# Kernel tuning notes

Hardware: AMD Instinct MI355X
Metric: run time of the kernel (lower is better)

Reference implementation:

```python
import jax, jax.numpy as jnp
import numpy as np
import math

B, S, D, H = 4, 2048, 1024, 16
HD = D // H
WINDOW = 86400.0 * 7.0  # 7 days, per create_time_mask(window_size=...)


def setup_inputs() -> dict:
    key = jax.random.key(0)
    ks = jax.random.split(key, 12)
    x = jax.random.normal(ks[0], (B, S, D), dtype=jnp.float32)
    # transaction timestamps: uniform over 30 days, sorted per sequence
    timestamps = jnp.sort(jax.random.uniform(ks[1], (B, S), dtype=jnp.float32) * (86400.0 * 30.0), axis=-1)
    init = 0.02
    Wq = jax.random.normal(ks[2], (D, D), dtype=jnp.float32) * init
    bq = jnp.zeros((D,), dtype=jnp.float32)
    Wk = jax.random.normal(ks[3], (D, D), dtype=jnp.float32) * init
    bk = jnp.zeros((D,), dtype=jnp.float32)
    Wv = jax.random.normal(ks[4], (D, D), dtype=jnp.float32) * init
    bv = jnp.zeros((D,), dtype=jnp.float32)
    Wo = jax.random.normal(ks[5], (D, D), dtype=jnp.float32) * init
    bo = jnp.zeros((D,), dtype=jnp.float32)
    Wc = jax.random.normal(ks[6], (1, D), dtype=jnp.float32) * init
    bc = jnp.zeros((1,), dtype=jnp.float32)
    return {"x": x, "timestamps": timestamps, "Wq": Wq, "bq": bq, "Wk": Wk, "bk": bk,
            "Wv": Wv, "bv": bv, "Wo": Wo, "bo": bo, "Wc": Wc, "bc": bc}


def reference(x, timestamps, Wq, bq, Wk, bk, Wv, bv, Wo, bo, Wc, bc):
    b, s, d = x.shape
    scale = 1.0 / math.sqrt(HD)
    # projections (torch Linear: y = x @ W.T + b), split heads -> [b, s, H, HD]
    Q = (x @ Wq.T + bq).reshape(b, s, H, HD)
    K = (x @ Wk.T + bk).reshape(b, s, H, HD)
    V = (x @ Wv.T + bv).reshape(b, s, H, HD)
    # scores [b, H, q, k]
    scores = jnp.einsum('bqhd,bkhd->bhqk', Q, K) * scale
    # time-window mask: attend only within +/- WINDOW seconds
    time_mask = jnp.abs(timestamps[:, :, None] - timestamps[:, None, :]) <= WINDOW  # [b, s, s]
    scores = jnp.where(time_mask[:, None, :, :], scores, -jnp.inf)
    attn = jax.nn.softmax(scores, axis=-1)
    attended = jnp.einsum('bhqk,bkhd->bqhd', attn, V).reshape(b, s, d)
    output = attended @ Wo.T + bo
    change_scores = (output @ Wc.T + bc)[..., 0]  # [b, s]
    return output, change_scores
```

## Files before the change

kernel.cpp:

```cpp
#include <hip/hip_runtime.h>
#include <math.h>

#define BB 4
#define SS 2048
#define DD 1024
#define HH 16
#define HDD 64
#define NN (BB*SS)
#define WINDOWF 604800.0f
#define LOG2E 1.44269504088896340736f
#define SCALE2 (0.125f * LOG2E)
#define MSTATIC 24.0f

typedef __attribute__((ext_vector_type(8))) short bf16x8;
typedef __attribute__((ext_vector_type(4))) short bf16x4;
typedef __attribute__((ext_vector_type(4))) short s16x4;
typedef __attribute__((ext_vector_type(4))) float f32x4;

__device__ __forceinline__ unsigned short f2b(float f) {
    unsigned int x = __float_as_uint(f);
    unsigned int r = x + 0x7FFFu + ((x >> 16) & 1u);
    return (unsigned short)(r >> 16);
}

__device__ __forceinline__ unsigned int cvt_pk_bf16(float lo, float hi) {
    unsigned int r;
    asm("v_cvt_pk_bf16_f32 %0, %1, %2" : "=v"(r) : "v"(lo), "v"(hi));
    return r;
}

__device__ __forceinline__ void gload16(const unsigned short* g, unsigned short* l) {
    __builtin_amdgcn_global_load_lds(
        (const __attribute__((address_space(1))) unsigned int*)g,
        (__attribute__((address_space(3))) unsigned int*)l, 16, 0, 0);
}

__global__ __launch_bounds__(256)
void cvt_band(const float* __restrict__ x,
              const float* __restrict__ Wq, const float* __restrict__ Wk,
              const float* __restrict__ Wv, const float* __restrict__ Wo,
              const float* __restrict__ ts, const float* __restrict__ bc,
              unsigned short* __restrict__ xb,
              unsigned short* __restrict__ Wqb, unsigned short* __restrict__ Wkb,
              unsigned short* __restrict__ Wvb, unsigned short* __restrict__ Wob,
              int* __restrict__ lo, int* __restrict__ hi,
              float* __restrict__ cs)
{
    const int g = blockIdx.x;
    const int tid = threadIdx.x;
    if (g < 12288) {
        const float* src; unsigned short* dst; int i;
        if (g < 8192) { src = x; dst = xb; i = g * 1024 + tid * 4; }
        else {
            const int wi = (g - 8192) >> 10;
            src = (wi == 0) ? Wq : (wi == 1) ? Wk : (wi == 2) ? Wv : Wo;
            dst = (wi == 0) ? Wqb : (wi == 1) ? Wkb : (wi == 2) ? Wvb : Wob;
            i = ((g - 8192) & 1023) * 1024 + tid * 4;
        }
        float4 v = *(const float4*)(src + i);
        s16x4 o;
        o[0] = (short)f2b(v.x); o[1] = (short)f2b(v.y);
        o[2] = (short)f2b(v.z); o[3] = (short)f2b(v.w);
        *(s16x4*)(dst + i) = o;
    } else if (g < 12320) {
        const int idx = (g - 12288) * 256 + tid;
        const int b = idx / SS, q = idx % SS;
        const float* t = ts + (size_t)b * SS;
        float tq = t[q];
        float lot = tq - WINDOWF - 1.0f;
        float hit = tq + WINDOWF + 1.0f;
        int l = 0, r = q;
        while (l < r) { int m = (l + r) >> 1; if (t[m] < lot) l = m + 1; else r = m; }
        lo[idx] = l;
        int l2 = q, r2 = SS - 1;
        while (l2 < r2) { int m = (l2 + r2 + 1) >> 1; if (t[m] > hit) r2 = m - 1; else l2 = m; }
        hi[idx] = l2;
    } else {
        const int i = (g - 12320) * 1024 + tid * 4;
        const float b0 = bc[0];
        float4 v = {b0, b0, b0, b0};
        *(float4*)(cs + i) = v;
    }
}

template<int OUTMODE>
__global__ __launch_bounds__(256)
void gemm_bf16(const unsigned short* __restrict__ A,
               const unsigned short* __restrict__ Bw,
               const float* __restrict__ bias,
               void* __restrict__ Y, int M, int N, int K, float alpha)
{
    constexpr int BM = 128, BN = 128, BK = 64;
    __shared__ unsigned short As[BM * BK];
    __shared__ unsigned short Bs[BN * BK];

    const int bm = blockIdx.x * BM;
    const int bn = blockIdx.y * BN;
    const int tid = threadIdx.x;
    const int wid = tid >> 6, l = tid & 63;
    const int wm = (wid >> 1) * 64, wn = (wid & 1) * 64;
    const int lr = l & 15, lg = l >> 4;

    const int srow = l >> 3;
    const int schunk = ((l & 7) ^ srow) * 8;

    f32x4 acc[4][4];
#pragma unroll
    for (int i = 0; i < 4; ++i)
#pragma unroll
        for (int j = 0; j < 4; ++j) acc[i][j] = (f32x4){0.f, 0.f, 0.f, 0.f};

    for (int k0 = 0; k0 < K; k0 += BK) {
#pragma unroll
        for (int i = 0; i < 4; ++i) {
            const int r0 = wid * 32 + i * 8;
            gload16(A  + (size_t)(bm + r0 + srow) * K + k0 + schunk, &As[r0 * BK]);
            gload16(Bw + (size_t)(bn + r0 + srow) * K + k0 + schunk, &Bs[r0 * BK]);
        }
        __syncthreads();

#pragma unroll
        for (int ks = 0; ks < 2; ++ks) {
            bf16x8 af[4], bf[4];
#pragma unroll
            for (int am = 0; am < 4; ++am) {
                const int row = wm + am * 16 + lr;
                af[am] = *(const bf16x8*)&As[row * BK + (((ks * 4 + lg) ^ (row & 7)) * 8)];
            }
#pragma unroll
            for (int nf = 0; nf < 4; ++nf) {
                const int row = wn + nf * 16 + lr;
                bf[nf] = *(const bf16x8*)&Bs[row * BK + (((ks * 4 + lg) ^ (row & 7)) * 8)];
            }
#pragma unroll
            for (int am = 0; am < 4; ++am)
#pragma unroll
                for (int nf = 0; nf < 4; ++nf)
                    acc[am][nf] = __builtin_amdgcn_mfma_f32_16x16x32_bf16(
                        af[am], bf[nf], acc[am][nf], 0, 0, 0);
        }
        __syncthreads();
    }

    float bia[4];
#pragma unroll
    for (int nf = 0; nf < 4; ++nf) bia[nf] = bias[bn + wn + nf * 16 + lr];

#pragma unroll
    for (int am = 0; am < 4; ++am)
#pragma unroll
        for (int nf = 0; nf < 4; ++nf) {
            if (OUTMODE == 2) {
                int mbase = bm + wm + am * 16 + lg * 4;
                int n = bn + wn + nf * 16 + lr;
                int bidx = mbase >> 11, sidx = mbase & (SS - 1);
                s16x4 o;
#pragma unroll
                for (int r = 0; r < 4; ++r)
                    o[r] = (short)f2b((acc[am][nf][r] + bia[nf]) * alpha);
                *(s16x4*)((unsigned short*)Y +
                          (((size_t)(bidx << 10) + n) << 11) + sidx) = o;
            } else {
#pragma unroll
                for (int r = 0; r < 4; ++r) {
                    float o = (acc[am][nf][r] + bia[nf]) * alpha;
                    size_t m = (size_t)(bm + wm + am * 16 + lg * 4 + r);
                    size_t n = (size_t)(bn + wn + nf * 16 + lr);
                    ((unsigned short*)Y)[m * N + n] = f2b(o);
                }
            }
        }
}

__global__ __launch_bounds__(256)
void gemm_wo_change(const unsigned short* __restrict__ A,
                    const unsigned short* __restrict__ Bw,
                    const float* __restrict__ bias,
                    float* __restrict__ Y,
                    const float* __restrict__ Wc,
                    float* __restrict__ cs)
{
    constexpr int BM = 128, BN = 128, BK = 64;
    __shared__ unsigned short As[BM * BK];
    __shared__ unsigned short Bs[BN * BK];

    const int bm = blockIdx.x * BM;
    const int bn = blockIdx.y * BN;
    const int tid = threadIdx.x;
    const int wid = tid >> 6, l = tid & 63;
    const int wm = (wid >> 1) * 64, wn = (wid & 1) * 64;
    const int lr = l & 15, lg = l >> 4;

    const int srow = l >> 3;
    const int schunk = ((l & 7) ^ srow) * 8;

    f32x4 acc[4][4];
#pragma unroll
    for (int i = 0; i < 4; ++i)
#pragma unroll
        for (int j = 0; j < 4; ++j) acc[i][j] = (f32x4){0.f, 0.f, 0.f, 0.f};

    for (int k0 = 0; k0 < DD; k0 += BK) {
#pragma unroll
        for (int i = 0; i < 4; ++i) {
            const int r0 = wid * 32 + i * 8;
            gload16(A  + (size_t)(bm + r0 + srow) * DD + k0 + schunk, &As[r0 * BK]);
            gload16(Bw + (size_t)(bn + r0 + srow) * DD + k0 + schunk, &Bs[r0 * BK]);
        }
        __syncthreads();

#pragma unroll
        for (int ks = 0; ks < 2; ++ks) {
            bf16x8 af[4], bf[4];
#pragma unroll
            for (int am = 0; am < 4; ++am) {
                const int row = wm + am * 16 + lr;
                af[am] = *(const bf16x8*)&As[row * BK + (((ks * 4 + lg) ^ (row & 7)) * 8)];
            }
#pragma unroll
            for (int nf = 0; nf < 4; ++nf) {
                const int row = wn + nf * 16 + lr;
                bf[nf] = *(const bf16x8*)&Bs[row * BK + (((ks * 4 + lg) ^ (row & 7)) * 8)];
            }
#pragma unroll
            for (int am = 0; am < 4; ++am)
#pragma unroll
                for (int nf = 0; nf < 4; ++nf)
                    acc[am][nf] = __builtin_amdgcn_mfma_f32_16x16x32_bf16(
                        af[am], bf[nf], acc[am][nf], 0, 0, 0);
        }
        __syncthreads();
    }

    float bia[4], wcv[4];
#pragma unroll
    for (int nf = 0; nf < 4; ++nf) {
        bia[nf] = bias[bn + wn + nf * 16 + lr];
        wcv[nf] = Wc[bn + wn + nf * 16 + lr];
    }

    float csum[4][4];
#pragma unroll
    for (int am = 0; am < 4; ++am)
#pragma unroll
        for (int r = 0; r < 4; ++r) csum[am][r] = 0.f;

#pragma unroll
    for (int am = 0; am < 4; ++am)
#pragma unroll
        for (int nf = 0; nf < 4; ++nf)
#pragma unroll
            for (int r = 0; r < 4; ++r) {
                float o = acc[am][nf][r] + bia[nf];
                size_t m = (size_t)(bm + wm + am * 16 + lg * 4 + r);
                size_t n = (size_t)(bn + wn + nf * 16 + lr);
                Y[m * DD + n] = o;
                csum[am][r] = fmaf(o, wcv[nf], csum[am][r]);
            }

#pragma unroll
    for (int am = 0; am < 4; ++am)
#pragma unroll
        for (int r = 0; r < 4; ++r) {
            float v = csum[am][r];
            v += __shfl_xor(v, 1);
            v += __shfl_xor(v, 2);
            v += __shfl_xor(v, 4);
            v += __shfl_xor(v, 8);
            if (lr == 0)
                atomicAdd(&cs[bm + wm + am * 16 + lg * 4 + r], v);
        }
}

__global__ __launch_bounds__(256)
void attn_mfma(const unsigned short* __restrict__ Qb, const unsigned short* __restrict__ Kb,
               const unsigned short* __restrict__ Vt, const float* __restrict__ Tg,
               const int* __restrict__ lo, const int* __restrict__ hi,
               unsigned short* __restrict__ Ab)
{
    __shared__ unsigned short Ks[2][64 * 64];
    __shared__ unsigned short Vs[2][64 * 64];

    const int blk = blockIdx.x;
    const int xcd = blk & 7;
    const int idx = blk >> 3;
    const int bh  = xcd * 8 + (idx >> 5);
    const int qt  = idx & 31;
    const int b = bh >> 4, h = bh & 15;

    const int tid = threadIdx.x;
    const int wid = tid >> 6, l = tid & 63;
    const int lr = l & 15, lg = l >> 4;
    const int q0w = qt * 64 + wid * 16;

    const size_t qrow = (size_t)(b * SS + q0w + lr);
    const bf16x8 qf0 = *(const bf16x8*)(Qb + qrow * DD + h * HDD + lg * 8);
    const bf16x8 qf1 = *(const bf16x8*)(Qb + qrow * DD + h * HDD + 32 + lg * 8);

    const float* tb = Tg + (size_t)b * SS;
    const float tq = tb[q0w + lr];
    const float tq_min = tb[qt * 64];
    const float tq_max = tb[qt * 64 + 63];

    const int t0 = lo[b * SS + qt * 64] >> 6;
    const int t1 = hi[b * SS + qt * 64 + 63] >> 6;

    const unsigned short* Kbh = Kb + (size_t)b * SS * DD + h * HDD;
    const unsigned short* Vth = Vt + ((size_t)(b * 1024 + h * HDD)) * SS;

    const int srow = l >> 3;
    const int schunk = (((l & 7) - srow) & 7) * 8;

    const unsigned short* kg0 = Kbh + (size_t)(t0 * 64 + wid * 16 + srow) * DD + schunk;
    const unsigned short* kg1 = kg0 + 8 * DD;
    const unsigned short* vg0 = Vth + (size_t)(wid * 16 + srow) * SS + t0 * 64 + schunk;
    const unsigned short* vg1 = vg0 + 8 * SS;

    const int ka_off = lr * 64 + (((lg + lr) & 7) << 3);
    const int c0 = lg >> 1, h4 = (lg & 1) * 4;
    const int pv0 = lr * 64 + (((c0 + 0 + lr) & 7) << 3) + h4;
    const int pv1 = lr * 64 + (((c0 + 2 + lr) & 7) << 3) + h4;
    const int pv2 = lr * 64 + (((c0 + 4 + lr) & 7) << 3) + h4;
    const int pv3 = lr * 64 + (((c0 + 6 + lr) & 7) << 3) + h4;

    bf16x8 onesv;
#pragma unroll
    for (int j = 0; j < 8; ++j) onesv[j] = (short)0x3F80;

    unsigned short *Kc = &Ks[0][0], *Kn = &Ks[1][0];
    unsigned short *Vc = &Vs[0][0], *Vn = &Vs[1][0];

    float l_ = 0.f;
    f32x4 o_[4];
#pragma unroll
    for (int df = 0; df < 4; ++df) o_[df] = (f32x4){0.f, 0.f, 0.f, 0.f};

    gload16(kg0, Kc + wid * 1024);
    gload16(kg1, Kc + wid * 1024 + 512);
    gload16(vg0, Vc + wid * 1024);
    gload16(vg1, Vc + wid * 1024 + 512);
    kg0 += 64 * DD; kg1 += 64 * DD; vg0 += 64; vg1 += 64;
    __syncthreads();

    for (int t = t0; t <= t1; ++t) {
        const int kk0 = t * 64;

        if (t < t1) {
            gload16(kg0, Kn + wid * 1024);
            gload16(kg1, Kn + wid * 1024 + 512);
            gload16(vg0, Vn + wid * 1024);
            gload16(vg1, Vn + wid * 1024 + 512);
            kg0 += 64 * DD; kg1 += 64 * DD; vg0 += 64; vg1 += 64;
        }

        f32x4 s[4];
        __builtin_amdgcn_s_setprio(1);
#pragma unroll
        for (int kf = 0; kf < 4; ++kf) {
            bf16x8 ka0 = *(const bf16x8*)(Kc + kf * 1024 + ka_off);
            bf16x8 ka1 = *(const bf16x8*)(Kc + kf * 1024 + (ka_off ^ 32));
            f32x4 z = (f32x4){-MSTATIC, -MSTATIC, -MSTATIC, -MSTATIC};
            z = __builtin_amdgcn_mfma_f32_16x16x32_bf16(ka0, qf0, z, 0, 0, 0);
            z = __builtin_amdgcn_mfma_f32_16x16x32_bf16(ka1, qf1, z, 0, 0, 0);
            s[kf] = z;
        }
        __builtin_amdgcn_s_setprio(0);

        const bool needmask = !((tq_max - tb[kk0] <= WINDOWF - 4.0f) &&
                                (tb[kk0 + 63] - tq_min <= WINDOWF - 4.0f));
        if (needmask) {
#pragma unroll
            for (int kf = 0; kf < 4; ++kf) {
                float4 tk4 = *(const float4*)(tb + kk0 + kf * 16 + lg * 4);
                if (!(fabsf(tq - tk4.x) <= WINDOWF)) s[kf][0] = -INFINITY;
                if (!(fabsf(tq - tk4.y) <= WINDOWF)) s[kf][1] = -INFINITY;
                if (!(fabsf(tq - tk4.z) <= WINDOWF)) s[kf][2] = -INFINITY;
                if (!(fabsf(tq - tk4.w) <= WINDOWF)) s[kf][3] = -INFINITY;
            }
        }

#pragma unroll
        for (int kf = 0; kf < 4; ++kf)
#pragma unroll
            for (int r = 0; r < 4; ++r)
                s[kf][r] = __builtin_amdgcn_exp2f(s[kf][r]);

        union { unsigned int u[4]; bf16x8 v; } pb[2];
#pragma unroll
        for (int c = 0; c < 2; ++c) {
            pb[c].u[0] = cvt_pk_bf16(s[2 * c][0],     s[2 * c][1]);
            pb[c].u[1] = cvt_pk_bf16(s[2 * c][2],     s[2 * c][3]);
            pb[c].u[2] = cvt_pk_bf16(s[2 * c + 1][0], s[2 * c + 1][1]);
            pb[c].u[3] = cvt_pk_bf16(s[2 * c + 1][2], s[2 * c + 1][3]);
        }

        __builtin_amdgcn_s_setprio(1);
        {
            f32x4 zl = (f32x4){0.f, 0.f, 0.f, 0.f};
            zl = __builtin_amdgcn_mfma_f32_16x16x32_bf16(onesv, pb[0].v, zl, 0, 0, 0);
            zl = __builtin_amdgcn_mfma_f32_16x16x32_bf16(onesv, pb[1].v, zl, 0, 0, 0);
            l_ += zl[0];
        }

#pragma unroll
        for (int df = 0; df < 4; ++df) {
            const int base = df * 1024;
            union { bf16x4 hh[2]; bf16x8 v; } va0, va1;
            va0.hh[0] = *(const bf16x4*)(Vc + base + pv0);
            va0.hh[1] = *(const bf16x4*)(Vc + base + pv1);
            va1.hh[0] = *(const bf16x4*)(Vc + base + pv2);
            va1.hh[1] = *(const bf16x4*)(Vc + base + pv3);
            o_[df] = __builtin_amdgcn_mfma_f32_16x16x32_bf16(va0.v, pb[0].v, o_[df], 0, 0, 0);
            o_[df] = __builtin_amdgcn_mfma_f32_16x16x32_bf16(va1.v, pb[1].v, o_[df], 0, 0, 0);
        }
        __builtin_amdgcn_s_setprio(0);

        __syncthreads();
        unsigned short* tk = Kc; Kc = Kn; Kn = tk;
        unsigned short* tv = Vc; Vc = Vn; Vn = tv;
    }

    const float inv = 1.f / l_;
#pragma unroll
    for (int df = 0; df < 4; ++df) {
        s16x4 o;
#pragma unroll
        for (int r = 0; r < 4; ++r) o[r] = (short)f2b(o_[df][r] * inv);
        *(s16x4*)(Ab + qrow * DD + h * HDD + df * 16 + lg * 4) = o;
    }
}

extern "C" void kernel_launch(void* const* d_in, const int* in_sizes, int n_in,
                              void* d_out, int out_size, void* d_ws, size_t ws_size,
                              hipStream_t stream)
{
    (void)in_sizes; (void)n_in; (void)out_size; (void)ws_size;
    const float* x  = (const float*)d_in[0];
    const float* ts = (const float*)d_in[1];
    const float* Wq = (const float*)d_in[2];
    const float* bq = (const float*)d_in[3];
    const float* Wk = (const float*)d_in[4];
    const float* bk = (const float*)d_in[5];
    const float* Wv = (const float*)d_in[6];
    const float* bv = (const float*)d_in[7];
    const float* Wo = (const float*)d_in[8];
    const float* bo = (const float*)d_in[9];
    const float* Wc = (const float*)d_in[10];
    const float* bc = (const float*)d_in[11];

    float* out = (float*)d_out;
    float* cs  = out + (size_t)NN * DD;

    unsigned short* xb  = (unsigned short*)d_ws;
    unsigned short* Qb  = xb  + (size_t)NN * DD;
    unsigned short* Kb2 = Qb  + (size_t)NN * DD;
    unsigned short* Vtb = Kb2 + (size_t)NN * DD;
    unsigned short* Abf = Vtb + (size_t)NN * DD;
    unsigned short* Wqb = Abf + (size_t)NN * DD;
    unsigned short* Wkb = Wqb + (size_t)DD * DD;
    unsigned short* Wvb = Wkb + (size_t)DD * DD;
    unsigned short* Wob = Wvb + (size_t)DD * DD;
    int* lo = (int*)(Wob + (size_t)DD * DD);
    int* hi = lo + NN;

    cvt_band<<<12328, 256, 0, stream>>>(x, Wq, Wk, Wv, Wo, ts, bc,
                                        xb, Wqb, Wkb, Wvb, Wob, lo, hi, cs);

    dim3 g(NN / 128, DD / 128);
    gemm_bf16<1><<<g, 256, 0, stream>>>(xb, Wqb, bq, Qb,  NN, DD, DD, SCALE2);
    gemm_bf16<1><<<g, 256, 0, stream>>>(xb, Wkb, bk, Kb2, NN, DD, DD, 1.0f);
    gemm_bf16<2><<<g, 256, 0, stream>>>(xb, Wvb, bv, Vtb, NN, DD, DD, 1.0f);
    attn_mfma<<<BB * HH * (SS / 64), 256, 0, stream>>>(Qb, Kb2, Vtb, ts, lo, hi, Abf);
    gemm_wo_change<<<g, 256, 0, stream>>>(Abf, Wob, bo, out, Wc, cs);
}
```

Measured before the change: 177.7 us.

## Merge Q/K projection launches, widen conversion vectors, reorder attention tile scheduling

The fp32-to-bf16 conversion now handles 8 elements per thread with 16-byte stores, which halves its block count. The Q and K projection GEMMs are merged into one launch with twice the grid, so there is one fewer launch and better occupancy. The shared GEMM main loop is factored into a device helper. Attention query tiles are interleaved outward from the middle of each sequence, which changes the order blocks are dispatched in and is meant to balance band-limited work. The gains are mostly launch-overhead and scheduling effects, and each one is small.

```diff
diff --git a/kernel.cpp b/kernel.cpp
--- a/kernel.cpp
+++ b/kernel.cpp
@@ -48,22 +48,25 @@
 {
     const int g = blockIdx.x;
     const int tid = threadIdx.x;
-    if (g < 12288) {
+    if (g < 6144) {
         const float* src; unsigned short* dst; int i;
-        if (g < 8192) { src = x; dst = xb; i = g * 1024 + tid * 4; }
+        if (g < 4096) { src = x; dst = xb; i = g * 2048 + tid * 8; }
         else {
-            const int wi = (g - 8192) >> 10;
+            const int wi = (g - 4096) >> 9;
             src = (wi == 0) ? Wq : (wi == 1) ? Wk : (wi == 2) ? Wv : Wo;
             dst = (wi == 0) ? Wqb : (wi == 1) ? Wkb : (wi == 2) ? Wvb : Wob;
-            i = ((g - 8192) & 1023) * 1024 + tid * 4;
-        }
-        float4 v = *(const float4*)(src + i);
-        s16x4 o;
-        o[0] = (short)f2b(v.x); o[1] = (short)f2b(v.y);
-        o[2] = (short)f2b(v.z); o[3] = (short)f2b(v.w);
-        *(s16x4*)(dst + i) = o;
-    } else if (g < 12320) {
-        const int idx = (g - 12288) * 256 + tid;
+            i = ((g - 4096) & 511) * 2048 + tid * 8;
+        }
+        float4 v0 = *(const float4*)(src + i);
+        float4 v1 = *(const float4*)(src + i + 4);
+        bf16x8 o;
+        o[0] = (short)f2b(v0.x); o[1] = (short)f2b(v0.y);
+        o[2] = (short)f2b(v0.z); o[3] = (short)f2b(v0.w);
+        o[4] = (short)f2b(v1.x); o[5] = (short)f2b(v1.y);
+        o[6] = (short)f2b(v1.z); o[7] = (short)f2b(v1.w);
+        *(bf16x8*)(dst + i) = o;
+    } else if (g < 6176) {
+        const int idx = (g - 6144) * 256 + tid;
         const int b = idx / SS, q = idx % SS;
         const float* t = ts + (size_t)b * SS;
         float tq = t[q];
@@ -76,26 +79,20 @@
         while (l2 < r2) { int m = (l2 + r2 + 1) >> 1; if (t[m] > hit) r2 = m - 1; else l2 = m; }
         hi[idx] = l2;
     } else {
-        const int i = (g - 12320) * 1024 + tid * 4;
+        const int i = (g - 6176) * 1024 + tid * 4;
         const float b0 = bc[0];
         float4 v = {b0, b0, b0, b0};
         *(float4*)(cs + i) = v;
     }
 }
 
-template<int OUTMODE>
-__global__ __launch_bounds__(256)
-void gemm_bf16(const unsigned short* __restrict__ A,
+__device__ __forceinline__
+void gemm_core(const unsigned short* __restrict__ A,
                const unsigned short* __restrict__ Bw,
-               const float* __restrict__ bias,
-               void* __restrict__ Y, int M, int N, int K, float alpha)
-{
-    constexpr int BM = 128, BN = 128, BK = 64;
-    __shared__ unsigned short As[BM * BK];
-    __shared__ unsigned short Bs[BN * BK];
-
-    const int bm = blockIdx.x * BM;
-    const int bn = blockIdx.y * BN;
+               int bm, int bn, int K,
+               unsigned short* As, unsigned short* Bs, f32x4 (&acc)[4][4])
+{
+    constexpr int BK = 64;
     const int tid = threadIdx.x;
     const int wid = tid >> 6, l = tid & 63;
     const int wm = (wid >> 1) * 64, wn = (wid & 1) * 64;
@@ -104,12 +101,6 @@
     const int srow = l >> 3;
     const int schunk = ((l & 7) ^ srow) * 8;
 
-    f32x4 acc[4][4];
-#pragma unroll
-    for (int i = 0; i < 4; ++i)
-#pragma unroll
-        for (int j = 0; j < 4; ++j) acc[i][j] = (f32x4){0.f, 0.f, 0.f, 0.f};
-
     for (int k0 = 0; k0 < K; k0 += BK) {
 #pragma unroll
         for (int i = 0; i < 4; ++i) {
@@ -141,7 +132,37 @@
         }
         __syncthreads();
     }
-
+}
+
+__global__ __launch_bounds__(256)
+void gemm_qk(const unsigned short* __restrict__ xb,
+             const unsigned short* __restrict__ Wqb,
+             const unsigned short* __restrict__ Wkb,
+             const float* __restrict__ bq, const float* __restrict__ bk,
+             unsigned short* __restrict__ Qb, unsigned short* __restrict__ Kb2)
+{
+    __shared__ unsigned short As[128 * 64];
+    __shared__ unsigned short Bs[128 * 64];
+
+    const int seg = blockIdx.y >> 3;
+    const int bm = blockIdx.x * 128;
+    const int bn = (blockIdx.y & 7) * 128;
+    const unsigned short* Bw = seg ? Wkb : Wqb;
+    const float* bias = seg ? bk : bq;
+    unsigned short* Y = seg ? Kb2 : Qb;
+    const float alpha = seg ? 1.0f : SCALE2;
+
+    f32x4 acc[4][4];
+#pragma unroll
+    for (int i = 0; i < 4; ++i)
+#pragma unroll
+        for (int j = 0; j < 4; ++j) acc[i][j] = (f32x4){0.f, 0.f, 0.f, 0.f};
+
+    gemm_core(xb, Bw, bm, bn, DD, As, Bs, acc);
+
+    const int l = threadIdx.x & 63, wid = threadIdx.x >> 6;
+    const int wm = (wid >> 1) * 64, wn = (wid & 1) * 64;
+    const int lr = l & 15, lg = l >> 4;
     float bia[4];
 #pragma unroll
     for (int nf = 0; nf < 4; ++nf) bia[nf] = bias[bn + wn + nf * 16 + lr];
@@ -149,26 +170,54 @@
 #pragma unroll
     for (int am = 0; am < 4; ++am)
 #pragma unroll
+        for (int nf = 0; nf < 4; ++nf)
+#pragma unroll
+            for (int r = 0; r < 4; ++r) {
+                float o = (acc[am][nf][r] + bia[nf]) * alpha;
+                size_t m = (size_t)(bm + wm + am * 16 + lg * 4 + r);
+                size_t n = (size_t)(bn + wn + nf * 16 + lr);
+                Y[m * DD + n] = f2b(o);
+            }
+}
+
+__global__ __launch_bounds__(256)
+void gemm_v(const unsigned short* __restrict__ xb,
+            const unsigned short* __restrict__ Wvb,
+            const float* __restrict__ bv, unsigned short* __restrict__ Vtb)
+{
+    __shared__ unsigned short As[128 * 64];
+    __shared__ unsigned short Bs[128 * 64];
+
+    const int bm = blockIdx.x * 128;
+    const int bn = blockIdx.y * 128;
+
+    f32x4 acc[4][4];
+#pragma unroll
+    for (int i = 0; i < 4; ++i)
+#pragma unroll
+        for (int j = 0; j < 4; ++j) acc[i][j] = (f32x4){0.f, 0.f, 0.f, 0.f};
+
+    gemm_core(xb, Wvb, bm, bn, DD, As, Bs, acc);
+
+    const int l = threadIdx.x & 63, wid = threadIdx.x >> 6;
+    const int wm = (wid >> 1) * 64, wn = (wid & 1) * 64;
+    const int lr = l & 15, lg = l >> 4;
+    float bia[4];
+#pragma unroll
+    for (int nf = 0; nf < 4; ++nf) bia[nf] = bv[bn + wn + nf * 16 + lr];
+
+#pragma unroll
+    for (int am = 0; am < 4; ++am)
+#pragma unroll
         for (int nf = 0; nf < 4; ++nf) {
-            if (OUTMODE == 2) {
-                int mbase = bm + wm + am * 16 + lg * 4;
-                int n = bn + wn + nf * 16 + lr;
-                int bidx = mbase >> 11, sidx = mbase & (SS - 1);
-                s16x4 o;
-#pragma unroll
-                for (int r = 0; r < 4; ++r)
-                    o[r] = (short)f2b((acc[am][nf][r] + bia[nf]) * alpha);
-                *(s16x4*)((unsigned short*)Y +
-                          (((size_t)(bidx << 10) + n) << 11) + sidx) = o;
-            } else {
-#pragma unroll
-                for (int r = 0; r < 4; ++r) {
-                    float o = (acc[am][nf][r] + bia[nf]) * alpha;
-                    size_t m = (size_t)(bm + wm + am * 16 + lg * 4 + r);
-                    size_t n = (size_t)(bn + wn + nf * 16 + lr);
-                    ((unsigned short*)Y)[m * N + n] = f2b(o);
-                }
-            }
+            int mbase = bm + wm + am * 16 + lg * 4;
+            int n = bn + wn + nf * 16 + lr;
+            int bidx = mbase >> 11, sidx = mbase & (SS - 1);
+            s16x4 o;
+#pragma unroll
+            for (int r = 0; r < 4; ++r)
+                o[r] = (short)f2b(acc[am][nf][r] + bia[nf]);
+            *(s16x4*)(Vtb + (((size_t)(bidx << 10) + n) << 11) + sidx) = o;
         }
 }
 
@@ -180,57 +229,23 @@
                     const float* __restrict__ Wc,
                     float* __restrict__ cs)
 {
-    constexpr int BM = 128, BN = 128, BK = 64;
-    __shared__ unsigned short As[BM * BK];
-    __shared__ unsigned short Bs[BN * BK];
-
-    const int bm = blockIdx.x * BM;
-    const int bn = blockIdx.y * BN;
-    const int tid = threadIdx.x;
-    const int wid = tid >> 6, l = tid & 63;
+    __shared__ unsigned short As[128 * 64];
+    __shared__ unsigned short Bs[128 * 64];
+
+    const int bm = blockIdx.x * 128;
+    const int bn = blockIdx.y * 128;
+
+    f32x4 acc[4][4];
+#pragma unroll
+    for (int i = 0; i < 4; ++i)
+#pragma unroll
+        for (int j = 0; j < 4; ++j) acc[i][j] = (f32x4){0.f, 0.f, 0.f, 0.f};
+
+    gemm_core(A, Bw, bm, bn, DD, As, Bs, acc);
+
+    const int l = threadIdx.x & 63, wid = threadIdx.x >> 6;
     const int wm = (wid >> 1) * 64, wn = (wid & 1) * 64;
     const int lr = l & 15, lg = l >> 4;
-
-    const int srow = l >> 3;
-    const int schunk = ((l & 7) ^ srow) * 8;
-
-    f32x4 acc[4][4];
-#pragma unroll
-    for (int i = 0; i < 4; ++i)
-#pragma unroll
-        for (int j = 0; j < 4; ++j) acc[i][j] = (f32x4){0.f, 0.f, 0.f, 0.f};
-
-    for (int k0 = 0; k0 < DD; k0 += BK) {
-#pragma unroll
-        for (int i = 0; i < 4; ++i) {
-            const int r0 = wid * 32 + i * 8;
-            gload16(A  + (size_t)(bm + r0 + srow) * DD + k0 + schunk, &As[r0 * BK]);
-            gload16(Bw + (size_t)(bn + r0 + srow) * DD + k0 + schunk, &Bs[r0 * BK]);
-        }
-        __syncthreads();
-
-#pragma unroll
-        for (int ks = 0; ks < 2; ++ks) {
-            bf16x8 af[4], bf[4];
-#pragma unroll
-            for (int am = 0; am < 4; ++am) {
-                const int row = wm + am * 16 + lr;
-                af[am] = *(const bf16x8*)&As[row * BK + (((ks * 4 + lg) ^ (row & 7)) * 8)];
-            }
-#pragma unroll
-            for (int nf = 0; nf < 4; ++nf) {
-                const int row = wn + nf * 16 + lr;
-                bf[nf] = *(const bf16x8*)&Bs[row * BK + (((ks * 4 + lg) ^ (row & 7)) * 8)];
-            }
-#pragma unroll
-            for (int am = 0; am < 4; ++am)
-#pragma unroll
-                for (int nf = 0; nf < 4; ++nf)
-                    acc[am][nf] = __builtin_amdgcn_mfma_f32_16x16x32_bf16(
-                        af[am], bf[nf], acc[am][nf], 0, 0, 0);
-        }
-        __syncthreads();
-    }
 
     float bia[4], wcv[4];
 #pragma unroll
@@ -285,7 +300,8 @@
     const int xcd = blk & 7;
     const int idx = blk >> 3;
     const int bh  = xcd * 8 + (idx >> 5);
-    const int qt  = idx & 31;
+    const int i5  = idx & 31;
+    const int qt  = (i5 & 1) ? (15 - (i5 >> 1)) : (16 + (i5 >> 1));
     const int b = bh >> 4, h = bh & 15;
 
     const int tid = threadIdx.x;
@@ -463,13 +479,12 @@
     int* lo = (int*)(Wob + (size_t)DD * DD);
     int* hi = lo + NN;
 
-    cvt_band<<<12328, 256, 0, stream>>>(x, Wq, Wk, Wv, Wo, ts, bc,
-                                        xb, Wqb, Wkb, Wvb, Wob, lo, hi, cs);
-
-    dim3 g(NN / 128, DD / 128);
-    gemm_bf16<1><<<g, 256, 0, stream>>>(xb, Wqb, bq, Qb,  NN, DD, DD, SCALE2);
-    gemm_bf16<1><<<g, 256, 0, stream>>>(xb, Wkb, bk, Kb2, NN, DD, DD, 1.0f);
-    gemm_bf16<2><<<g, 256, 0, stream>>>(xb, Wvb, bv, Vtb, NN, DD, DD, 1.0f);
+    cvt_band<<<6184, 256, 0, stream>>>(x, Wq, Wk, Wv, Wo, ts, bc,
+                                       xb, Wqb, Wkb, Wvb, Wob, lo, hi, cs);
+
+    gemm_qk<<<dim3(NN / 128, 16), 256, 0, stream>>>(xb, Wqb, Wkb, bq, bk, Qb, Kb2);
+    gemm_v<<<dim3(NN / 128, DD / 128), 256, 0, stream>>>(xb, Wvb, bv, Vtb);
+
     attn_mfma<<<BB * HH * (SS / 64), 256, 0, stream>>>(Qb, Kb2, Vtb, ts, lo, hi, Abf);
-    gemm_wo_change<<<g, 256, 0, stream>>>(Abf, Wob, bo, out, Wc, cs);
-}
+    gemm_wo_change<<<dim3(NN / 128, DD / 128), 256, 0, stream>>>(Abf, Wob, bo, out, Wc, cs);
+}
```

After: 171.5 us (median of 3 runs). -3.5%, faster.
